# Performance work log

Measured on AMD Instinct MI355X. Metric: run time of the kernel, lower is better.

Reference implementation:

```python
import jax, jax.numpy as jnp
import numpy as np

N_HEADS = 16
HEAD_DIM = 64
D_MODEL = 1024

def setup_inputs() -> dict:
    key = jax.random.key(0)
    k1, k2, k3 = jax.random.split(key, 3)
    B, S = 4, 2048
    x = jax.random.normal(k1, (B, S, D_MODEL), dtype=jnp.float32)
    Wqkv = jax.random.normal(k2, (D_MODEL, 3 * D_MODEL), dtype=jnp.float32) * (D_MODEL ** -0.5)
    bqkv = jnp.zeros((3 * D_MODEL,), dtype=jnp.float32)
    Wo = jax.random.normal(k3, (D_MODEL, D_MODEL), dtype=jnp.float32) * (D_MODEL ** -0.5)
    bo = jnp.zeros((D_MODEL,), dtype=jnp.float32)
    return {"x": x, "Wqkv": Wqkv, "bqkv": bqkv, "Wo": Wo, "bo": bo}

def reference(x, Wqkv, bqkv, Wo, bo):
    B, S, E = x.shape
    H, D = N_HEADS, HEAD_DIM
    qkv = x @ Wqkv + bqkv                      # [B,S,3E]
    q, k, v = jnp.split(qkv, 3, axis=-1)
    q = q.reshape(B, S, H, D).transpose(0, 2, 1, 3)  # [B,H,S,D]
    k = k.reshape(B, S, H, D).transpose(0, 2, 1, 3)
    v = v.reshape(B, S, H, D).transpose(0, 2, 1, 3)
    scores = jnp.einsum('bhsd,bhtd->bhst', q, k) / jnp.sqrt(jnp.float32(D))
    causal = jnp.tril(jnp.ones((S, S), dtype=bool))
    scores = jnp.where(causal[None, None], scores, jnp.float32(-jnp.inf))
    attn = jax.nn.softmax(scores, axis=-1)
    y = jnp.einsum('bhst,bhtd->bhsd', attn, v)       # [B,H,S,D]
    y = y.transpose(0, 2, 1, 3).reshape(B, S, E)
    return y @ Wo + bo
```

## Files before the change

kernel.cpp:

```cpp
#include <hip/hip_runtime.h>
#include <hip/hip_bf16.h>
#include <stdint.h>

typedef __bf16 bf16;
typedef __bf16 bf16x8 __attribute__((ext_vector_type(8)));
typedef __bf16 bf16x4 __attribute__((ext_vector_type(4)));
typedef float  f32x4  __attribute__((ext_vector_type(4)));
typedef float  f32x16 __attribute__((ext_vector_type(16)));
typedef unsigned u32x2 __attribute__((ext_vector_type(2)));

__device__ __forceinline__ void load_lds16(const void* g, void* l) {
  __builtin_amdgcn_global_load_lds((const __attribute__((address_space(1))) void*)g,
                                   (__attribute__((address_space(3))) void*)l, 16, 0, 0);
}

__device__ __forceinline__ unsigned pk2(float a, float b) {
  union { bf16 h[2]; unsigned u; } t;
  t.h[0] = (bf16)a; t.h[1] = (bf16)b;
  return t.u;
}

__global__ __launch_bounds__(256) void f32_to_bf16_k(const float* __restrict__ in,
                                                     bf16* __restrict__ out) {
  int i = (blockIdx.x * 256 + threadIdx.x) * 8;
  float4 a = *(const float4*)(in + i);
  float4 b = *(const float4*)(in + i + 4);
  bf16x8 o;
  o[0] = (bf16)a.x; o[1] = (bf16)a.y; o[2] = (bf16)a.z; o[3] = (bf16)a.w;
  o[4] = (bf16)b.x; o[5] = (bf16)b.y; o[6] = (bf16)b.z; o[7] = (bf16)b.w;
  *(bf16x8*)(out + i) = o;
}

__global__ __launch_bounds__(256) void transpose_to_bf16_k(const float* __restrict__ in,
                                                           bf16* __restrict__ out,
                                                           int K, int N) {
  __shared__ __align__(16) bf16 tile[64 * 72];
  int n0 = blockIdx.x * 64, k0 = blockIdx.y * 64;
  int t = threadIdx.x;
  int r = t >> 2, cq = (t & 3) * 16;
  const float* src = in + (size_t)(k0 + r) * N + n0 + cq;
#pragma unroll
  for (int j = 0; j < 16; j += 4) {
    float4 v = *(const float4*)(src + j);
    tile[r * 72 + cq + j + 0] = (bf16)v.x;
    tile[r * 72 + cq + j + 1] = (bf16)v.y;
    tile[r * 72 + cq + j + 2] = (bf16)v.z;
    tile[r * 72 + cq + j + 3] = (bf16)v.w;
  }
  __syncthreads();
  bf16x8 r0, r1;
#pragma unroll
  for (int j = 0; j < 8; ++j) r0[j] = tile[(cq + j) * 72 + r];
#pragma unroll
  for (int j = 0; j < 8; ++j) r1[j] = tile[(cq + 8 + j) * 72 + r];
  bf16* dst = out + (size_t)(n0 + r) * K + k0 + cq;
  *(bf16x8*)(dst) = r0;
  *(bf16x8*)(dst + 8) = r1;
}

template <int EPI>
__global__ __launch_bounds__(256) void gemm_bt(const bf16* __restrict__ A,
                                               const bf16* __restrict__ BT,
                                               const float* __restrict__ bias,
                                               float* __restrict__ Cf,
                                               bf16* __restrict__ qk,
                                               bf16* __restrict__ vt,
                                               int M, int N, int K) {
  __shared__ __align__(16) bf16 As[128 * 64];
  __shared__ __align__(16) bf16 Bs[128 * 64];
  const int tid = threadIdx.x;
  const int w = tid >> 6, l = tid & 63;
  const int g = l >> 4, c = l & 15;
  const int wm = w >> 1, wn = w & 1;
  const int brow = blockIdx.y * 128;
  const int bcol = blockIdx.x * 128;
  const int lr = l >> 3;
  const int lg = l & 7;

  f32x4 acc[4][4];
#pragma unroll
  for (int m = 0; m < 4; ++m)
#pragma unroll
    for (int n = 0; n < 4; ++n) acc[m][n] = f32x4{0.f, 0.f, 0.f, 0.f};

  const int nkt = K >> 6;
  for (int kt = 0; kt < nkt; ++kt) {
    if (kt) __syncthreads();
    const int k0 = kt * 64;
#pragma unroll
    for (int i = 0; i < 4; ++i) {
      int row = w * 32 + i * 8 + lr;
      int src_k = k0 + ((lg ^ (row & 7)) * 8);
      load_lds16(A + (size_t)(brow + row) * K + src_k, &As[(w * 32 + i * 8) * 64]);
      load_lds16(BT + (size_t)(bcol + row) * K + src_k, &Bs[(w * 32 + i * 8) * 64]);
    }
    asm volatile("s_waitcnt vmcnt(0)" ::: "memory");
    __syncthreads();

#pragma unroll
    for (int ks = 0; ks < 2; ++ks) {
      bf16x8 af[4], bfr[4];
#pragma unroll
      for (int m = 0; m < 4; ++m)
        af[m] = *(const bf16x8*)&As[(wm * 64 + m * 16 + c) * 64 + (((ks * 4 + g) ^ (c & 7)) * 8)];
#pragma unroll
      for (int n = 0; n < 4; ++n)
        bfr[n] = *(const bf16x8*)&Bs[(wn * 64 + n * 16 + c) * 64 + (((ks * 4 + g) ^ (c & 7)) * 8)];
#pragma unroll
      for (int m = 0; m < 4; ++m)
#pragma unroll
        for (int n = 0; n < 4; ++n)
          acc[m][n] = __builtin_amdgcn_mfma_f32_16x16x32_bf16(af[m], bfr[n], acc[m][n], 0, 0, 0);
    }
  }

#pragma unroll
  for (int m = 0; m < 4; ++m) {
    int row_l = wm * 64 + m * 16 + (l >> 4) * 4;
#pragma unroll
    for (int n = 0; n < 4; ++n) {
      int col = bcol + wn * 64 + n * 16 + c;
      float bv = bias[col];
      if (EPI == 0) {
        if (bcol < 2048) {
#pragma unroll
          for (int r = 0; r < 4; ++r) {
            int row = brow + row_l + r;
            qk[(size_t)row * 2048 + col] = (bf16)(acc[m][n][r] + bv);
          }
        } else {
          int hh = (col - 2048) >> 6, dd = (col - 2048) & 63;
          int row0 = brow + row_l;
          int bb = row0 >> 11, ss = row0 & 2047;
          bf16x4 pk;
#pragma unroll
          for (int r = 0; r < 4; ++r) pk[r] = (bf16)(acc[m][n][r] + bv);
          *(bf16x4*)&vt[((size_t)(bb * 16 + hh) * 64 + dd) * 2048 + ss] = pk;
        }
      } else {
#pragma unroll
        for (int r = 0; r < 4; ++r) {
          int row = brow + row_l + r;
          Cf[(size_t)row * N + col] = acc[m][n][r] + bv;
        }
      }
    }
  }
}

__global__ __launch_bounds__(128) void attn_k(const bf16* __restrict__ qkbuf,
                                              const bf16* __restrict__ vtbuf,
                                              bf16* __restrict__ aout) {
  __shared__ __align__(16) bf16 Ks[2][64 * 64];
  __shared__ __align__(16) bf16 Vs[2][64 * 64];

  const int tid = threadIdx.x;
  const int w = tid >> 6, l = tid & 63;
  const int c32 = l & 31, hi = l >> 5;

  const int bid = blockIdx.x;
  const int xcd = bid & 7;
  const int idx = bid >> 3;
  const int bh = xcd * 8 + (idx >> 4);
  const int j = idx & 15;
  const int p = j >> 1, h0 = j & 1;
  const int b = bh >> 4, h = bh & 15;

  const bf16* ksrc = qkbuf + (size_t)(b * 2048) * 2048 + 1024 + h * 64;
  const bf16* vsrc = vtbuf + (size_t)(bh * 64) * 2048;

#pragma unroll 1
  for (int item = 0; item < 2; ++item) {
    const int qblk = item == 0 ? 15 - p : p;
    const int half = item == 0 ? h0 : 1 - h0;
    const int nt = 2 * qblk + half + 1;
    const int qw = qblk * 128 + half * 64 + w * 32;
    const int myq = qw + c32;

    const size_t qoff = (size_t)(b * 2048 + myq) * 2048 + h * 64;
    bf16x8 qf[4];
#pragma unroll
    for (int t = 0; t < 4; ++t) {
      bf16x8 v = *(const bf16x8*)&qkbuf[qoff + t * 16 + hi * 8];
#pragma unroll
      for (int jj = 0; jj < 8; ++jj) v[jj] = (bf16)((float)v[jj] * 0.125f);
      qf[t] = v;
    }

    float m_r = -1e30f, l_r = 0.f;
    f32x16 o[2];
    o[0] = (f32x16)(0.f); o[1] = (f32x16)(0.f);

#define STAGE_TILE(buf, KV0)                                                        \
    {                                                                               \
      const int kv0s = (KV0);                                                       \
      _Pragma("unroll")                                                             \
      for (int i = 0; i < 4; ++i) {                                                 \
        int rr = w * 32 + i * 8 + (l >> 3);                                         \
        int sw = ((l & 7) ^ (rr & 7)) * 8;                                          \
        load_lds16(ksrc + (size_t)(kv0s + rr) * 2048 + sw,                          \
                   &Ks[buf][(w * 32 + i * 8) * 64]);                                \
        load_lds16(vsrc + (size_t)rr * 2048 + kv0s + sw,                            \
                   &Vs[buf][(w * 32 + i * 8) * 64]);                                \
      }                                                                             \
    }

    STAGE_TILE(0, 0)
    asm volatile("s_waitcnt vmcnt(0)" ::: "memory");
    __syncthreads();

    int cur = 0;
    for (int kt = 0; kt < nt; ++kt) {
      const int kv0 = kt * 64;
      if (kt + 1 < nt) STAGE_TILE(cur ^ 1, kv0 + 64)

      const bf16* kb = &Ks[cur][0];
      const bf16* vb = &Vs[cur][0];

      f32x16 st[2];
      st[0] = (f32x16)(0.f); st[1] = (f32x16)(0.f);
      __builtin_amdgcn_s_setprio(1);
#pragma unroll
      for (int t = 0; t < 4; ++t) {
#pragma unroll
        for (int ks = 0; ks < 2; ++ks) {
          int kv = ks * 32 + c32;
          bf16x8 kf = *(const bf16x8*)&kb[kv * 64 + (((2 * t + hi) ^ (kv & 7)) * 8)];
          st[ks] = __builtin_amdgcn_mfma_f32_32x32x16_bf16(kf, qf[t], st[ks], 0, 0, 0);
        }
      }
      __builtin_amdgcn_s_setprio(0);

      if (kv0 + 63 > qw) {
#pragma unroll
        for (int ks = 0; ks < 2; ++ks)
#pragma unroll
          for (int r = 0; r < 16; ++r) {
            int kvidx = kv0 + ks * 32 + (r & 3) + 8 * (r >> 2) + 4 * hi;
            if (kvidx > myq) st[ks][r] = -1e30f;
          }
      }

      float t0[8];
#pragma unroll
      for (int i = 0; i < 8; ++i)
        t0[i] = fmaxf(fmaxf(st[0][i], st[0][i + 8]), fmaxf(st[1][i], st[1][i + 8]));
      float mx = fmaxf(fmaxf(fmaxf(t0[0], t0[1]), fmaxf(t0[2], t0[3])),
                       fmaxf(fmaxf(t0[4], t0[5]), fmaxf(t0[6], t0[7])));
      {
        u32x2 mres = __builtin_amdgcn_permlane32_swap(__float_as_uint(mx),
                                                      __float_as_uint(mx), false, false);
        mx = fmaxf(__uint_as_float(mres[0]), __uint_as_float(mres[1]));
      }

      if (__any(mx > m_r + 8.0f)) {
        float mn = fmaxf(m_r, mx);
        float al = __expf(m_r - mn);
        m_r = mn;
        l_r *= al;
#pragma unroll
        for (int ds = 0; ds < 2; ++ds)
#pragma unroll
          for (int r = 0; r < 16; ++r) o[ds][r] *= al;
      }

      float s0 = 0.f, s1 = 0.f, s2 = 0.f, s3 = 0.f;
#pragma unroll
      for (int ks = 0; ks < 2; ++ks)
#pragma unroll
        for (int r = 0; r < 16; r += 4) {
          float p0 = __expf(st[ks][r + 0] - m_r);
          float p1 = __expf(st[ks][r + 1] - m_r);
          float p2 = __expf(st[ks][r + 2] - m_r);
          float p3 = __expf(st[ks][r + 3] - m_r);
          st[ks][r + 0] = p0; st[ks][r + 1] = p1;
          st[ks][r + 2] = p2; st[ks][r + 3] = p3;
          s0 += p0; s1 += p1; s2 += p2; s3 += p3;
        }
      float ps = (s0 + s1) + (s2 + s3);
      {
        u32x2 sres = __builtin_amdgcn_permlane32_swap(__float_as_uint(ps),
                                                      __float_as_uint(ps), false, false);
        ps = __uint_as_float(sres[0]) + __uint_as_float(sres[1]);
      }
      l_r += ps;

      bf16x8 pfr[4];
#pragma unroll
      for (int t = 0; t < 4; ++t) {
        const int ks = t >> 1, eb = (t & 1) * 8;
        unsigned w0 = pk2(st[ks][eb + 0], st[ks][eb + 1]);
        unsigned w1 = pk2(st[ks][eb + 2], st[ks][eb + 3]);
        unsigned w2 = pk2(st[ks][eb + 4], st[ks][eb + 5]);
        unsigned w3 = pk2(st[ks][eb + 6], st[ks][eb + 7]);
        u32x2 r02 = __builtin_amdgcn_permlane32_swap(w0, w2, false, false);
        u32x2 r13 = __builtin_amdgcn_permlane32_swap(w1, w3, false, false);
        union { unsigned u[4]; bf16x8 v; } pf;
        pf.u[0] = r02[0]; pf.u[1] = r13[0]; pf.u[2] = r02[1]; pf.u[3] = r13[1];
        pfr[t] = pf.v;
      }

      __builtin_amdgcn_s_setprio(1);
#pragma unroll
      for (int t = 0; t < 4; ++t) {
#pragma unroll
        for (int ds = 0; ds < 2; ++ds) {
          int d = ds * 32 + c32;
          bf16x8 vf = *(const bf16x8*)&vb[d * 64 + (((2 * t + hi) ^ (d & 7)) * 8)];
          o[ds] = __builtin_amdgcn_mfma_f32_32x32x16_bf16(vf, pfr[t], o[ds], 0, 0, 0);
        }
      }
      __builtin_amdgcn_s_setprio(0);

      asm volatile("s_waitcnt vmcnt(0)" ::: "memory");
      __syncthreads();
      cur ^= 1;
    }

    const float inv = 1.0f / l_r;
    bf16* orow = aout + (size_t)(b * 2048 + myq) * 1024 + h * 64;
#pragma unroll
    for (int ds = 0; ds < 2; ++ds)
#pragma unroll
      for (int rg = 0; rg < 4; ++rg) {
        bf16x4 pk;
#pragma unroll
        for (int i = 0; i < 4; ++i) pk[i] = (bf16)(o[ds][rg * 4 + i] * inv);
        *(bf16x4*)&orow[ds * 32 + rg * 8 + hi * 4] = pk;
      }
#undef STAGE_TILE
  }
}

extern "C" void kernel_launch(void* const* d_in, const int* in_sizes, int n_in,
                              void* d_out, int out_size, void* d_ws, size_t ws_size,
                              hipStream_t stream) {
  const float* x    = (const float*)d_in[0];
  const float* Wqkv = (const float*)d_in[1];
  const float* bqkv = (const float*)d_in[2];
  const float* Wo   = (const float*)d_in[3];
  const float* bo   = (const float*)d_in[4];
  float* out = (float*)d_out;

  char* ws = (char*)d_ws;
  bf16* xb   = (bf16*)(ws);
  bf16* wqt  = (bf16*)(ws + 16777216);
  bf16* wot  = (bf16*)(ws + 23068672);
  bf16* qkb  = (bf16*)(ws + 25165824);
  bf16* vtb  = (bf16*)(ws + 58720256);
  bf16* aob  = (bf16*)(ws + 75497472);

  f32_to_bf16_k<<<dim3(4096), dim3(256), 0, stream>>>(x, xb);
  transpose_to_bf16_k<<<dim3(48, 16), dim3(256), 0, stream>>>(Wqkv, wqt, 1024, 3072);
  transpose_to_bf16_k<<<dim3(16, 16), dim3(256), 0, stream>>>(Wo, wot, 1024, 1024);
  gemm_bt<0><<<dim3(24, 64), dim3(256), 0, stream>>>(xb, wqt, bqkv, nullptr, qkb, vtb,
                                                     8192, 3072, 1024);
  attn_k<<<dim3(1024), dim3(128), 0, stream>>>(qkb, vtb, aob);
  gemm_bt<1><<<dim3(8, 64), dim3(256), 0, stream>>>(aob, wot, bo, out, nullptr, nullptr,
                                                    8192, 1024, 1024);
}
```

Before: 190.2 us.

## Add 256x256 double-buffered QKV GEMM kernel with XCD-aware block mapping

Replaces the 128x128-tile QKV projection GEMM with a dedicated 512-thread kernel that computes 256x256 tiles. It double-buffers LDS loads so the next K-slice is fetched while the current one runs through MFMA, and uses s_setprio around the MFMA bursts. Blocks are remapped so that each XCD works on a contiguous set of row tiles. The larger tiles are meant to raise data reuse and cut global traffic per FLOP. The cost is 128KB of LDS per block and heavy register pressure from 32 accumulators, which limits occupancy.

```diff
diff --git a/kernel.cpp b/kernel.cpp
--- a/kernel.cpp
+++ b/kernel.cpp
@@ -58,13 +58,120 @@
   *(bf16x8*)(dst + 8) = r1;
 }
 
-template <int EPI>
+__global__ __launch_bounds__(512, 2) void gemm1_256(const bf16* __restrict__ A,
+                                                    const bf16* __restrict__ BT,
+                                                    const float* __restrict__ bias,
+                                                    bf16* __restrict__ qk,
+                                                    bf16* __restrict__ vt) {
+  __shared__ __align__(16) bf16 As[2][256 * 64];
+  __shared__ __align__(16) bf16 Bs[2][256 * 64];
+  const int K = 1024;
+  const int tid = threadIdx.x;
+  const int w = tid >> 6, l = tid & 63;
+  const int g = l >> 4, c = l & 15;
+  const int wm = w >> 2, wn = w & 3;
+
+  const int bid = blockIdx.x;
+  const int xcd = bid & 7;
+  const int idx = bid >> 3;
+  const int by = xcd * 4 + idx / 12;
+  const int bx = idx % 12;
+  const int brow = by * 256;
+  const int bcol = bx * 256;
+
+  f32x4 acc[8][4];
+#pragma unroll
+  for (int m = 0; m < 8; ++m)
+#pragma unroll
+    for (int n = 0; n < 4; ++n) acc[m][n] = f32x4{0.f, 0.f, 0.f, 0.f};
+
+#define STAGE256(buf, K0)                                                          \
+  {                                                                                \
+    _Pragma("unroll")                                                              \
+    for (int i = 0; i < 4; ++i) {                                                  \
+      int rr = w * 32 + i * 8 + (l >> 3);                                          \
+      int sk = (K0) + (((l & 7) ^ (rr & 7)) * 8);                                  \
+      load_lds16(A + (size_t)(brow + rr) * K + sk, &As[buf][(w * 32 + i * 8) * 64]);\
+      load_lds16(BT + (size_t)(bcol + rr) * K + sk, &Bs[buf][(w * 32 + i * 8) * 64]);\
+    }                                                                              \
+  }
+
+  STAGE256(0, 0)
+  int cur = 0;
+  const int nkt = K >> 6;
+  for (int kt = 0; kt < nkt; ++kt) {
+    if (kt + 1 < nkt) {
+      STAGE256(cur ^ 1, (kt + 1) << 6)
+      asm volatile("s_waitcnt vmcnt(8)" ::: "memory");
+    } else {
+      asm volatile("s_waitcnt vmcnt(0)" ::: "memory");
+    }
+    __builtin_amdgcn_s_barrier();
+    __builtin_amdgcn_sched_barrier(0);
+
+    bf16x8 bfr[4];
+#pragma unroll
+    for (int p = 0; p < 4; ++p) {
+      const int ks = p >> 1, mh = p & 1;
+      if (mh == 0) {
+#pragma unroll
+        for (int n = 0; n < 4; ++n) {
+          int r = wn * 64 + n * 16 + c;
+          bfr[n] = *(const bf16x8*)&Bs[cur][r * 64 + (((ks * 4 + g) ^ (r & 7)) * 8)];
+        }
+      }
+      bf16x8 af[4];
+#pragma unroll
+      for (int m = 0; m < 4; ++m) {
+        int r = wm * 128 + mh * 64 + m * 16 + c;
+        af[m] = *(const bf16x8*)&As[cur][r * 64 + (((ks * 4 + g) ^ (r & 7)) * 8)];
+      }
+      __builtin_amdgcn_s_setprio(1);
+#pragma unroll
+      for (int m = 0; m < 4; ++m)
+#pragma unroll
+        for (int n = 0; n < 4; ++n)
+          acc[mh * 4 + m][n] =
+              __builtin_amdgcn_mfma_f32_16x16x32_bf16(af[m], bfr[n], acc[mh * 4 + m][n], 0, 0, 0);
+      __builtin_amdgcn_s_setprio(0);
+      __builtin_amdgcn_sched_barrier(0);
+    }
+    __builtin_amdgcn_s_barrier();
+    __builtin_amdgcn_sched_barrier(0);
+    cur ^= 1;
+  }
+#undef STAGE256
+
+#pragma unroll
+  for (int m = 0; m < 8; ++m) {
+    int row_l = wm * 128 + m * 16 + g * 4;
+#pragma unroll
+    for (int n = 0; n < 4; ++n) {
+      int col = bcol + wn * 64 + n * 16 + c;
+      float bv = bias[col];
+      if (col < 2048) {
+#pragma unroll
+        for (int r = 0; r < 4; ++r) {
+          int row = brow + row_l + r;
+          qk[(size_t)row * 2048 + col] = (bf16)(acc[m][n][r] + bv);
+        }
+      } else {
+        int hh = (col - 2048) >> 6, dd = (col - 2048) & 63;
+        int row0 = brow + row_l;
+        int bb = row0 >> 11, ss = row0 & 2047;
+        bf16x4 pk;
+#pragma unroll
+        for (int r = 0; r < 4; ++r) pk[r] = (bf16)(acc[m][n][r] + bv);
+        *(bf16x4*)&vt[((size_t)(bb * 16 + hh) * 64 + dd) * 2048 + ss] = pk;
+      }
+    }
+  }
+}
+
 __global__ __launch_bounds__(256) void gemm_bt(const bf16* __restrict__ A,
                                                const bf16* __restrict__ BT,
                                                const float* __restrict__ bias,
                                                float* __restrict__ Cf,
-                                               bf16* __restrict__ qk,
-                                               bf16* __restrict__ vt,
                                                int M, int N, int K) {
   __shared__ __align__(16) bf16 As[128 * 64];
   __shared__ __align__(16) bf16 Bs[128 * 64];
@@ -121,28 +228,10 @@
     for (int n = 0; n < 4; ++n) {
       int col = bcol + wn * 64 + n * 16 + c;
       float bv = bias[col];
-      if (EPI == 0) {
-        if (bcol < 2048) {
-#pragma unroll
-          for (int r = 0; r < 4; ++r) {
-            int row = brow + row_l + r;
-            qk[(size_t)row * 2048 + col] = (bf16)(acc[m][n][r] + bv);
-          }
-        } else {
-          int hh = (col - 2048) >> 6, dd = (col - 2048) & 63;
-          int row0 = brow + row_l;
-          int bb = row0 >> 11, ss = row0 & 2047;
-          bf16x4 pk;
-#pragma unroll
-          for (int r = 0; r < 4; ++r) pk[r] = (bf16)(acc[m][n][r] + bv);
-          *(bf16x4*)&vt[((size_t)(bb * 16 + hh) * 64 + dd) * 2048 + ss] = pk;
-        }
-      } else {
-#pragma unroll
-        for (int r = 0; r < 4; ++r) {
-          int row = brow + row_l + r;
-          Cf[(size_t)row * N + col] = acc[m][n][r] + bv;
-        }
+#pragma unroll
+      for (int r = 0; r < 4; ++r) {
+        int row = brow + row_l + r;
+        Cf[(size_t)row * N + col] = acc[m][n][r] + bv;
       }
     }
   }
@@ -353,9 +442,7 @@
   f32_to_bf16_k<<<dim3(4096), dim3(256), 0, stream>>>(x, xb);
   transpose_to_bf16_k<<<dim3(48, 16), dim3(256), 0, stream>>>(Wqkv, wqt, 1024, 3072);
   transpose_to_bf16_k<<<dim3(16, 16), dim3(256), 0, stream>>>(Wo, wot, 1024, 1024);
-  gemm_bt<0><<<dim3(24, 64), dim3(256), 0, stream>>>(xb, wqt, bqkv, nullptr, qkb, vtb,
-                                                     8192, 3072, 1024);
+  gemm1_256<<<dim3(384), dim3(512), 0, stream>>>(xb, wqt, bqkv, qkb, vtb);
   attn_k<<<dim3(1024), dim3(128), 0, stream>>>(qkb, vtb, aob);
-  gemm_bt<1><<<dim3(8, 64), dim3(256), 0, stream>>>(aob, wot, bo, out, nullptr, nullptr,
-                                                    8192, 1024, 1024);
-}
+  gemm_bt<<<dim3(8, 64), dim3(256), 0, stream>>>(aob, wot, bo, out, 8192, 1024, 1024);
+}
```

Result: slower. 197.1 us (+3.6%).
